# Optimization experiments

Measured on AMD Instinct MI355X. Metric: run time of the kernel, lower is better.

The kernel has to match this reference:

```python
import jax, jax.numpy as jnp
import numpy as np

# Norse default LIFParameters
TAU_SYN_INV = 200.0  # 1/5e-3
TAU_MEM_INV = 100.0  # 1/1e-2
V_LEAK = 0.0
V_TH = 1.0
V_RESET = 0.0
DT = 0.001


def _heaviside(x):
    return (x > 0).astype(x.dtype)


def setup_inputs() -> dict:
    key = jax.random.key(0)
    k1, k2 = jax.random.split(key)
    T, B, F = 1024, 256, 512
    input_spikes = (jax.random.uniform(k1, (T, B, F)) < 0.1).astype(jnp.float32)
    W = jax.random.normal(k2, (F, F), dtype=jnp.float32) / np.sqrt(F).astype(np.float32)
    return {"input_spikes": input_spikes, "W": W}


def reference(input_spikes, W):
    # input_spikes: [T, B, F]; W: [F, F] (Linear, no bias)
    T, B, F = input_spikes.shape
    # fc batched across the whole sequence (y = x @ W.T)
    xs = jnp.einsum('tbf,gf->tbg', input_spikes, W)  # [T, B, F]
    v0 = jnp.zeros((B, F), dtype=input_spikes.dtype)
    i0 = jnp.zeros((B, F), dtype=input_spikes.dtype)

    def step(carry, x):
        v, i = carry
        v_dec = v + DT * TAU_MEM_INV * ((V_LEAK - v) + i)  # membrane leak+integrate
        i_dec = i - DT * TAU_SYN_INV * i                   # synaptic current decay
        z = _heaviside(v_dec - V_TH)                       # spike
        v_new = (1.0 - z) * v_dec + z * V_RESET            # reset
        i_new = i_dec + x                                  # inject fc output
        return (v_new, i_new), z

    (v, i), zs = jax.lax.scan(step, (v0, i0), xs)
    # matches torch forward: returns (z_last, state) with state = (v, i)
    return zs[-1], v, i
```

## Files before the change

kernel.cpp:

```cpp
#include <hip/hip_runtime.h>
#include <hip/hip_bf16.h>


typedef __attribute__((ext_vector_type(8))) short short8;
typedef __attribute__((ext_vector_type(4))) float floatx4;
typedef __attribute__((ext_vector_type(2))) unsigned uintx2;
typedef __attribute__((ext_vector_type(4))) int int4v;

#define T_STEPS 1024
#define B_DIM   256
#define F_DIM   512
#define BF      (B_DIM * F_DIM)
#define ROWP    520

static __device__ __forceinline__ unsigned short f2bf_rne(float f) {
    unsigned u = __float_as_uint(f);
    return (unsigned short)((u + 0x7FFFu + ((u >> 16) & 1u)) >> 16);
}
static __device__ __forceinline__ float bf2f(unsigned short h) {
    return __uint_as_float(((unsigned)h) << 16);
}

__global__ __launch_bounds__(256)
void pack_kernel(const float* __restrict__ sp, unsigned* __restrict__ bits)
{
    const int lane = threadIdx.x & 63;
    const int wv   = blockIdx.x * 4 + (threadIdx.x >> 6);
    for (int c = wv; c < 65536; c += 2048 * 4) {
        const float* p = sp + (size_t)c * 2048;
        unsigned val = 0;
        #pragma unroll
        for (int r = 0; r < 32; ++r) {
            float x = p[r * 64 + lane];
            unsigned long long m = __ballot(x != 0.0f);
            unsigned sel = (lane & 1) ? (unsigned)(m >> 32) : (unsigned)m;
            if ((lane >> 1) == r) val = sel;
        }
        bits[(size_t)c * 64 + lane] = val;
    }
}

__global__ __launch_bounds__(512, 4)
void lif_kernel_bits(const unsigned* __restrict__ bits,
                     const float* __restrict__ W,
                     float* __restrict__ out)
{
    __shared__ int   xq[4][8 * 256];
    __shared__ float rowmax[8][16];

    const int tid  = threadIdx.x;
    const int lane = tid & 63;
    const int wq   = tid >> 6;
    const int bt   = blockIdx.x & 15;
    const int gb   = blockIdx.x >> 4;
    const int b0   = bt * 16;
    const int gw   = gb * 16;
    const int mrow = lane & 15;
    const int lq   = lane >> 4;

    int4v wi0, wi1, wi2;
    float invC;
    {
        const float* wp = W + (size_t)(gw + mrow) * F_DIM + wq * 64 + lq * 16;
        float wv[16];
        float lm = 0.0f;
        #pragma unroll
        for (int j = 0; j < 16; ++j) {
            wv[j] = wp[j];
            lm = fmaxf(lm, fabsf(wv[j]));
        }
        lm = fmaxf(lm, __shfl_xor(lm, 16, 64));
        lm = fmaxf(lm, __shfl_xor(lm, 32, 64));
        if (lane < 16) rowmax[wq][lane] = lm;
        __syncthreads();
        float S = 1e-30f;
        #pragma unroll
        for (int w8 = 0; w8 < 8; ++w8) S = fmaxf(S, rowmax[w8][mrow]);
        __syncthreads();
        const float C = 8000000.0f / S;
        invC = S / 8000000.0f;
        #pragma unroll
        for (int d = 0; d < 4; ++d) {
            unsigned p0 = 0, p1 = 0, p2 = 0;
            #pragma unroll
            for (int jj = 0; jj < 4; ++jj) {
                int q  = __float2int_rn(wv[d * 4 + jj] * C);
                int d2 = (q << 24) >> 24;
                int r1 = (q - d2) >> 8;
                int d1 = (r1 << 24) >> 24;
                int d0 = (r1 - d1) >> 8;
                p0 |= (unsigned)(d0 & 0xFF) << (8 * jj);
                p1 |= (unsigned)(d1 & 0xFF) << (8 * jj);
                p2 |= (unsigned)(d2 & 0xFF) << (8 * jj);
            }
            wi0[d] = (int)p0; wi1[d] = (int)p1; wi2[d] = (int)p2;
        }
    }

    const bool fin   = (wq < 2);
    const int  rbase = (wq & 1) * 2;
    float v0 = 0.f, v1 = 0.f, c0 = 0.f, c1 = 0.f, z0 = 0.f, z1 = 0.f;

    const unsigned* bp = bits + (size_t)(b0 + mrow) * 16 + wq * 2;

    auto ldbits = [&](int t) -> uintx2 {
        return *(const uintx2*)(bp + (size_t)t * 4096);
    };

    auto expand = [&](uintx2 bq) -> int4v {
        unsigned h16 = ((lq & 2) ? bq[1] : bq[0]) >> ((lq & 1) * 16);
        int4v a;
        #pragma unroll
        for (int d = 0; d < 4; ++d) {
            unsigned b4 = (h16 >> (4 * d)) & 0xFu;
            a[d] = (int)((b4 * 0x00204081u) & 0x01010101u);
        }
        return a;
    };

    const int4v iz = {0, 0, 0, 0};

    auto mci = [&](int4v aI) -> int4v {
        int4v a0 = __builtin_amdgcn_mfma_i32_16x16x64_i8(aI, wi0, iz, 0, 0, 0);
        int4v a1 = __builtin_amdgcn_mfma_i32_16x16x64_i8(aI, wi1, iz, 0, 0, 0);
        int4v a2 = __builtin_amdgcn_mfma_i32_16x16x64_i8(aI, wi2, iz, 0, 0, 0);
        int4v c;
        #pragma unroll
        for (int r = 0; r < 4; ++r)
            c[r] = ((a0[r] << 16) + (a1[r] << 8)) + a2[r];
        return c;
    };

    auto lif2 = [&](const int* xs) {
        int s0 = 0, s1 = 0;
        #pragma unroll
        for (int w8 = 0; w8 < 8; ++w8) {
            const int* p = xs + w8 * 256 + lane * 4 + rbase;
            s0 += p[0];
            s1 += p[1];
        }
        float x0 = (float)s0 * invC;
        float x1 = (float)s1 * invC;
        float vd0 = v0 + 0.1f * ((0.0f - v0) + c0);
        float id0 = c0 - 0.2f * c0;
        bool  sp0 = (vd0 - 1.0f) > 0.0f;
        z0 = sp0 ? 1.0f : 0.0f;
        v0 = sp0 ? 0.0f : vd0;
        c0 = id0 + x0;
        float vd1 = v1 + 0.1f * ((0.0f - v1) + c1);
        float id1 = c1 - 0.2f * c1;
        bool  sp1 = (vd1 - 1.0f) > 0.0f;
        z1 = sp1 ? 1.0f : 0.0f;
        v1 = sp1 ? 0.0f : vd1;
        c1 = id1 + x1;
    };

    uintx2 bqA = ldbits(0);
    uintx2 bqB = ldbits(1);

    for (int t = 0; t < T_STEPS; t += 2) {
        if (fin && t > 0) {
            lif2(&xq[(t + 2) & 3][0]);
            lif2(&xq[(t + 3) & 3][0]);
        }
        {
            int4v cA = mci(expand(bqA));
            *(int4v*)&xq[t & 3][wq * 256 + lane * 4] = cA;
            int4v cB = mci(expand(bqB));
            *(int4v*)&xq[(t + 1) & 3][wq * 256 + lane * 4] = cB;
        }
        if (t + 2 < T_STEPS) {
            bqA = ldbits(t + 2);
            bqB = ldbits(t + 3);
        }
        __syncthreads();
    }
    if (fin) {
        lif2(&xq[2][0]);
        lif2(&xq[3][0]);
        const int blo = b0 + lq * 4 + rbase;
        const int gg  = gw + mrow;
        {
            const size_t i0 = (size_t)blo * F_DIM + gg;
            out[i0]          = z0;
            out[BF + i0]     = v0;
            out[2 * BF + i0] = c0;
            const size_t i1 = (size_t)(blo + 1) * F_DIM + gg;
            out[i1]          = z1;
            out[BF + i1]     = v1;
            out[2 * BF + i1] = c1;
        }
    }
}

__global__ __launch_bounds__(256, 1)
void lif_kernel_f32(const float* __restrict__ spikes,
                    const float* __restrict__ W,
                    float* __restrict__ out)
{
    __shared__ unsigned short sAf[16 * ROWP];
    __shared__ float xbuf[2 * 256];

    const int tid  = threadIdx.x;
    const int lane = tid & 63;
    const int w    = tid >> 6;
    const int gh   = w & 1;
    const int kh   = w >> 1;
    const int bt   = blockIdx.x & 15;
    const int gb   = blockIdx.x >> 4;
    const int b0   = bt * 16;
    const int gw   = gb * 32 + gh * 16;
    const int mrow = lane & 15;
    const int kq   = lane >> 4;

    short8 whi[8], wmd[8], wlo[8];
    {
        const float* wp = W + (size_t)(gw + mrow) * F_DIM + kh * 256 + kq * 8;
        #pragma unroll
        for (int ks = 0; ks < 8; ++ks) {
            short8 hi, md, lo;
            #pragma unroll
            for (int j = 0; j < 8; ++j) {
                float f = wp[ks * 32 + j];
                unsigned short h = f2bf_rne(f);
                float r1 = f - bf2f(h);
                unsigned short m = f2bf_rne(r1);
                float r2 = r1 - bf2f(m);
                hi[j] = (short)h;
                md[j] = (short)m;
                lo[j] = (short)f2bf_rne(r2);
            }
            whi[ks] = hi; wmd[ks] = md; wlo[ks] = lo;
        }
    }

    float v[4]  = {0.f, 0.f, 0.f, 0.f};
    float cu[4] = {0.f, 0.f, 0.f, 0.f};
    float zf[4] = {0.f, 0.f, 0.f, 0.f};

    floatx4 ld[8];
    auto issue_loads = [&](int t) {
        const floatx4* sp = (const floatx4*)(spikes + (size_t)t * BF + (size_t)b0 * F_DIM);
        #pragma unroll
        for (int j = 0; j < 8; ++j)
            ld[j] = sp[tid + 256 * j];
    };

    issue_loads(0);
    for (int t = 0; t < T_STEPS; ++t) {
        #pragma unroll
        for (int j = 0; j < 8; ++j) {
            const int q = tid + 256 * j;
            const int row = q >> 7, col4 = q & 127;
            unsigned u0 = __float_as_uint(ld[j][0]);
            unsigned u1 = __float_as_uint(ld[j][1]);
            unsigned u2 = __float_as_uint(ld[j][2]);
            unsigned u3 = __float_as_uint(ld[j][3]);
            uintx2 d;
            d[0] = (u0 >> 16) | (u1 & 0xFFFF0000u);
            d[1] = (u2 >> 16) | (u3 & 0xFFFF0000u);
            *(uintx2*)&sAf[row * ROWP + col4 * 4] = d;
        }
        __syncthreads();
        if (t + 1 < T_STEPS) issue_loads(t + 1);

        floatx4 ah = {0.f, 0.f, 0.f, 0.f};
        floatx4 am = {0.f, 0.f, 0.f, 0.f};
        floatx4 al = {0.f, 0.f, 0.f, 0.f};
        const unsigned short* arow = &sAf[mrow * ROWP + kh * 256 + kq * 8];
        #pragma unroll
        for (int ks = 0; ks < 8; ++ks) {
            short8 a = *(const short8*)(arow + ks * 32);
            ah = __builtin_amdgcn_mfma_f32_16x16x32_bf16(a, whi[ks], ah, 0, 0, 0);
            am = __builtin_amdgcn_mfma_f32_16x16x32_bf16(a, wmd[ks], am, 0, 0, 0);
            al = __builtin_amdgcn_mfma_f32_16x16x32_bf16(a, wlo[ks], al, 0, 0, 0);
        }

        if (kh == 1) {
            floatx4 xp = (ah + am) + al;
            *(floatx4*)&xbuf[gh * 256 + lane * 4] = xp;
        }
        __syncthreads();
        if (kh == 0) {
            floatx4 other = *(const floatx4*)&xbuf[gh * 256 + lane * 4];
            #pragma unroll
            for (int r = 0; r < 4; ++r) {
                float x    = ((ah[r] + am[r]) + al[r]) + other[r];
                float vdec = v[r] + 0.1f * ((0.0f - v[r]) + cu[r]);
                float idec = cu[r] - 0.2f * cu[r];
                bool  spk  = (vdec - 1.0f) > 0.0f;
                zf[r] = spk ? 1.0f : 0.0f;
                v[r]  = spk ? 0.0f : vdec;
                cu[r] = idec + x;
            }
        }
    }

    if (kh == 0) {
        #pragma unroll
        for (int r = 0; r < 4; ++r) {
            const size_t idx = (size_t)(b0 + kq * 4 + r) * F_DIM + gw + mrow;
            out[idx]          = zf[r];
            out[BF + idx]     = v[r];
            out[2 * BF + idx] = cu[r];
        }
    }
}

extern "C" void kernel_launch(void* const* d_in, const int* in_sizes, int n_in,
                              void* d_out, int out_size, void* d_ws, size_t ws_size,
                              hipStream_t stream)
{
    const float* spikes = (const float*)d_in[0];
    const float* W      = (const float*)d_in[1];
    float* out          = (float*)d_out;

    const size_t need_bits = (size_t)T_STEPS * B_DIM * (F_DIM / 8);

    if (d_ws != nullptr && ws_size >= need_bits) {
        unsigned* bits = (unsigned*)d_ws;
        pack_kernel<<<dim3(2048), dim3(256), 0, stream>>>(spikes, bits);
        lif_kernel_bits<<<dim3(512), dim3(512), 0, stream>>>(bits, W, out);
    } else {
        lif_kernel_f32<<<dim3(256), dim3(256), 0, stream>>>(spikes, W, out);
    }
}
```

Measured before the change: 1.072 ms.

## Batch four timesteps per barrier and spread LIF update across four waves

Each loop iteration now processes four timesteps instead of two, using an 8-slot double-buffered shared partial-sum array, which halves the number of block barriers. The LIF recurrence is split across four waves, each owning one row, instead of two waves handling two rows each. Shared-memory layout changes to [slot][row][col] so reductions read contiguous lanes, and bit loads become single dwords per lane. In exchange, shared memory doubles (64KB of partials), which may limit occupancy at 4 blocks per CU.

```diff
diff --git a/kernel.cpp b/kernel.cpp
--- a/kernel.cpp
+++ b/kernel.cpp
@@ -45,7 +45,7 @@
                      const float* __restrict__ W,
                      float* __restrict__ out)
 {
-    __shared__ int   xq[4][8 * 256];
+    __shared__ int   xq[8][4][512];
     __shared__ float rowmax[8][16];
 
     const int tid  = threadIdx.x;
@@ -97,18 +97,19 @@
         }
     }
 
-    const bool fin   = (wq < 2);
-    const int  rbase = (wq & 1) * 2;
-    float v0 = 0.f, v1 = 0.f, c0 = 0.f, c1 = 0.f, z0 = 0.f, z1 = 0.f;
-
-    const unsigned* bp = bits + (size_t)(b0 + mrow) * 16 + wq * 2;
-
-    auto ldbits = [&](int t) -> uintx2 {
-        return *(const uintx2*)(bp + (size_t)t * 4096);
-    };
-
-    auto expand = [&](uintx2 bq) -> int4v {
-        unsigned h16 = ((lq & 2) ? bq[1] : bq[0]) >> ((lq & 1) * 16);
+    const bool fin  = (wq < 4);
+    const int  rown = wq & 3;
+    float v0 = 0.f, c0 = 0.f, z0 = 0.f;
+
+    const unsigned* bp = bits + (size_t)(b0 + mrow) * 16 + wq * 2 + (lq >> 1);
+    const int hsh = (lq & 1) * 16;
+
+    auto ldbits = [&](int t) -> unsigned {
+        return bp[(size_t)t * 4096];
+    };
+
+    auto expand = [&](unsigned dw) -> int4v {
+        unsigned h16 = dw >> hsh;
         int4v a;
         #pragma unroll
         for (int d = 0; d < 4; ++d) {
@@ -131,65 +132,65 @@
         return c;
     };
 
-    auto lif2 = [&](const int* xs) {
-        int s0 = 0, s1 = 0;
-        #pragma unroll
-        for (int w8 = 0; w8 < 8; ++w8) {
-            const int* p = xs + w8 * 256 + lane * 4 + rbase;
-            s0 += p[0];
-            s1 += p[1];
-        }
-        float x0 = (float)s0 * invC;
-        float x1 = (float)s1 * invC;
-        float vd0 = v0 + 0.1f * ((0.0f - v0) + c0);
-        float id0 = c0 - 0.2f * c0;
-        bool  sp0 = (vd0 - 1.0f) > 0.0f;
-        z0 = sp0 ? 1.0f : 0.0f;
-        v0 = sp0 ? 0.0f : vd0;
-        c0 = id0 + x0;
-        float vd1 = v1 + 0.1f * ((0.0f - v1) + c1);
-        float id1 = c1 - 0.2f * c1;
-        bool  sp1 = (vd1 - 1.0f) > 0.0f;
-        z1 = sp1 ? 1.0f : 0.0f;
-        v1 = sp1 ? 0.0f : vd1;
-        c1 = id1 + x1;
-    };
-
-    uintx2 bqA = ldbits(0);
-    uintx2 bqB = ldbits(1);
-
-    for (int t = 0; t < T_STEPS; t += 2) {
+    auto wrpart = [&](int slot, int4v c) {
+        #pragma unroll
+        for (int r = 0; r < 4; ++r)
+            xq[slot][r][wq * 64 + lane] = c[r];
+    };
+
+    auto lif1 = [&](int slot) {
+        const int* p = &xq[slot][rown][lane];
+        int s = 0;
+        #pragma unroll
+        for (int w8 = 0; w8 < 8; ++w8)
+            s += p[w8 * 64];
+        float x  = (float)s * invC;
+        float vd = v0 + 0.1f * ((0.0f - v0) + c0);
+        float id = c0 - 0.2f * c0;
+        bool  sp = (vd - 1.0f) > 0.0f;
+        z0 = sp ? 1.0f : 0.0f;
+        v0 = sp ? 0.0f : vd;
+        c0 = id + x;
+    };
+
+    unsigned q0 = ldbits(0), q1 = ldbits(1), q2 = ldbits(2), q3 = ldbits(3);
+
+    for (int t = 0; t < T_STEPS; t += 4) {
+        const int sw = t & 4;
+        const int sr = 4 - sw;
+
+        int4v aA = expand(q0);
+        int4v aB = expand(q1);
+        int4v aC = expand(q2);
+        int4v aD = expand(q3);
+        if (t + 4 < T_STEPS) {
+            q0 = ldbits(t + 4);
+            q1 = ldbits(t + 5);
+            q2 = ldbits(t + 6);
+            q3 = ldbits(t + 7);
+        }
+        wrpart(sw + 0, mci(aA));
+        wrpart(sw + 1, mci(aB));
+        wrpart(sw + 2, mci(aC));
+        wrpart(sw + 3, mci(aD));
+
         if (fin && t > 0) {
-            lif2(&xq[(t + 2) & 3][0]);
-            lif2(&xq[(t + 3) & 3][0]);
-        }
-        {
-            int4v cA = mci(expand(bqA));
-            *(int4v*)&xq[t & 3][wq * 256 + lane * 4] = cA;
-            int4v cB = mci(expand(bqB));
-            *(int4v*)&xq[(t + 1) & 3][wq * 256 + lane * 4] = cB;
-        }
-        if (t + 2 < T_STEPS) {
-            bqA = ldbits(t + 2);
-            bqB = ldbits(t + 3);
+            lif1(sr + 0);
+            lif1(sr + 1);
+            lif1(sr + 2);
+            lif1(sr + 3);
         }
         __syncthreads();
     }
     if (fin) {
-        lif2(&xq[2][0]);
-        lif2(&xq[3][0]);
-        const int blo = b0 + lq * 4 + rbase;
-        const int gg  = gw + mrow;
-        {
-            const size_t i0 = (size_t)blo * F_DIM + gg;
-            out[i0]          = z0;
-            out[BF + i0]     = v0;
-            out[2 * BF + i0] = c0;
-            const size_t i1 = (size_t)(blo + 1) * F_DIM + gg;
-            out[i1]          = z1;
-            out[BF + i1]     = v1;
-            out[2 * BF + i1] = c1;
-        }
+        lif1(4);
+        lif1(5);
+        lif1(6);
+        lif1(7);
+        const size_t idx = (size_t)(b0 + lq * 4 + rown) * F_DIM + gw + mrow;
+        out[idx]          = z0;
+        out[BF + idx]     = v0;
+        out[2 * BF + idx] = c0;
     }
 }
 
```

After: 1.144 ms. 1.07x slower.
